# Kernel optimization log

Measured on AMD Instinct MI355X. Metric: run time of the kernel, lower is better.

## Reference

```python
import jax, jax.numpy as jnp
import numpy as np

N_NODES = 50000
N_EDGES = 800000


def gcn_conv(x, edge_index, W, b):
    """PyG GCNConv: add self-loops, symmetric deg^{-1/2} normalization,
    dense transform, scatter-add aggregation."""
    n = x.shape[0]
    src, dst = edge_index[0], edge_index[1]
    # add self-loops
    loop = jnp.arange(n, dtype=src.dtype)
    src = jnp.concatenate([src, loop])
    dst = jnp.concatenate([dst, loop])
    # degree on destination nodes (includes self-loops -> deg >= 1)
    deg = jax.ops.segment_sum(jnp.ones_like(dst, dtype=x.dtype), dst, num_segments=n)
    dinv = jax.lax.rsqrt(deg)
    norm = dinv[src] * dinv[dst]  # [E+N]
    h = x @ W                     # [N, F_out] dense GEMM
    msg = h[src] * norm[:, None]  # gather + scale, [E+N, F_out]
    out = jax.ops.segment_sum(msg, dst, num_segments=n)  # scatter-add
    return out + b


def setup_inputs() -> dict:
    key = jax.random.key(0)
    ks = jax.random.split(key, 8)
    x = jax.random.normal(ks[0], (N_NODES, 100), dtype=jnp.float32)
    edge_index = jax.random.randint(ks[1], (2, N_EDGES), 0, N_NODES, dtype=jnp.int64)
    W1 = jax.random.normal(ks[2], (100, 256), dtype=jnp.float32) * 0.1
    b1 = jnp.zeros((256,), dtype=jnp.float32)
    W2 = jax.random.normal(ks[3], (256, 128), dtype=jnp.float32) * 0.06
    b2 = jnp.zeros((128,), dtype=jnp.float32)
    Wfc = jax.random.normal(ks[4], (128, 1), dtype=jnp.float32) * 0.09
    bfc = jnp.zeros((1,), dtype=jnp.float32)
    return {"x": x, "edge_index": edge_index, "W1": W1, "b1": b1,
            "W2": W2, "b2": b2, "Wfc": Wfc, "bfc": bfc}


def reference(x, edge_index, W1, b1, W2, b2, Wfc, bfc):
    # eval mode: F.dropout with training=False is identity
    h = jax.nn.relu(gcn_conv(x, edge_index, W1, b1))
    h = jax.nn.relu(gcn_conv(h, edge_index, W2, b2))
    return h @ Wfc + bfc  # [N, 1]
```

## Files before the change

### kernel.cpp

```cpp
#include <hip/hip_runtime.h>
#include <hip/hip_bf16.h>


#define F0 100
#define F1 256
#define F2 128

typedef _Float16 f16x4 __attribute__((ext_vector_type(4)));
typedef _Float16 f16x8 __attribute__((ext_vector_type(8)));
typedef float f32x4 __attribute__((ext_vector_type(4)));


__global__ void deg_count_i(const int* __restrict__ dst, int* deg, int e) {
    int i = blockIdx.x * blockDim.x + threadIdx.x;
    if (i < e) atomicAdd(deg + dst[i], 1);
}

__global__ __launch_bounds__(256) void scan1(const int* __restrict__ deg,
                                             int* __restrict__ excl,
                                             int* __restrict__ bsum,
                                             float* __restrict__ dinv, int n) {
    __shared__ int wsum[4];
    int i = blockIdx.x * 256 + threadIdx.x;
    int lane = threadIdx.x & 63, wid = threadIdx.x >> 6;
    int v = (i < n) ? deg[i] : 0;
    if (i < n) dinv[i] = rsqrtf((float)(v + 1));
    int s = v;
#pragma unroll
    for (int off = 1; off < 64; off <<= 1) {
        int t = __shfl_up(s, off, 64);
        if (lane >= off) s += t;
    }
    if (lane == 63) wsum[wid] = s;
    __syncthreads();
    int add = 0;
    for (int w = 0; w < wid; w++) add += wsum[w];
    if (i < n) excl[i] = add + s - v;
    if (threadIdx.x == 255) bsum[blockIdx.x] = add + s;
}

__global__ __launch_bounds__(256) void scan2(int* __restrict__ bsum, int nb,
                                             int* __restrict__ rowptr, int n) {
    __shared__ int wsum[4];
    int lane = threadIdx.x & 63, wid = threadIdx.x >> 6;
    int v = (threadIdx.x < nb) ? bsum[threadIdx.x] : 0;
    int s = v;
#pragma unroll
    for (int off = 1; off < 64; off <<= 1) {
        int t = __shfl_up(s, off, 64);
        if (lane >= off) s += t;
    }
    if (lane == 63) wsum[wid] = s;
    __syncthreads();
    int add = 0;
    for (int w = 0; w < wid; w++) add += wsum[w];
    if (threadIdx.x < nb) bsum[threadIdx.x] = add + s - v;
    if (threadIdx.x == 255) rowptr[n] = add + s;
}

__global__ void scan3(const int* __restrict__ excl, const int* __restrict__ bsum,
                      int* __restrict__ rowptr, int* __restrict__ cursor, int n) {
    int i = blockIdx.x * 256 + threadIdx.x;
    if (i < n) {
        int r = excl[i] + bsum[blockIdx.x];
        rowptr[i] = r;
        cursor[i] = r;
    }
}

__global__ void csr_fill(const int* __restrict__ src, const int* __restrict__ dst,
                         int* cursor, int* __restrict__ csr, int e) {
    int i = blockIdx.x * blockDim.x + threadIdx.x;
    if (i < e) {
        int pos = atomicAdd(cursor + dst[i], 1);
        csr[pos] = src[i];
    }
}

__global__ void scale_x(const float4* __restrict__ x4,
                        const float* __restrict__ dinv,
                        float4* __restrict__ xs4, int n25) {
    int i = blockIdx.x * blockDim.x + threadIdx.x;
    if (i < n25) {
        float d = dinv[i / 25];
        float4 v = x4[i];
        v.x *= d; v.y *= d; v.z *= d; v.w *= d;
        xs4[i] = v;
    }
}

__global__ void wprep(const float* __restrict__ W1, const float* __restrict__ W2,
                      _Float16* __restrict__ W1h, _Float16* __restrict__ W1l,
                      _Float16* __restrict__ W2h, _Float16* __restrict__ W2l) {
    int i = blockIdx.x * 256 + threadIdx.x;
    if (i < 256 * 128) {
        int c = i >> 7, k = i & 127;
        float v = (k < F0) ? W1[(size_t)k * F1 + c] : 0.f;
        _Float16 h = (_Float16)v;
        W1h[i] = h;
        W1l[i] = (_Float16)(v - (float)h);
    } else if (i < 256 * 128 + 128 * 256) {
        int j = i - 256 * 128;
        int c = j >> 8, k = j & 255;
        float v = W2[(size_t)k * F2 + c];
        _Float16 h = (_Float16)v;
        W2h[j] = h;
        W2l[j] = (_Float16)(v - (float)h);
    }
}


__global__ __launch_bounds__(256) void pull_f100(
        const float* __restrict__ xs, const int* __restrict__ rowptr,
        const int* __restrict__ csr, const float* __restrict__ dinv,
        _Float16* __restrict__ aggh, _Float16* __restrict__ aggl, int n) {
    int wave = threadIdx.x >> 6, lane = threadIdx.x & 63;
    int v = blockIdx.x * 4 + wave;
    if (v >= n) return;
    int beg = rowptr[v], end = rowptr[v + 1];
    float dv = dinv[v];
    int half = lane >> 5, q = lane & 31;
    bool act = q < 25;
    float4 acc = {0.f, 0.f, 0.f, 0.f};
    if (half == 0 && act) acc = ((const float4*)(xs + (size_t)v * F0))[q];

    for (int base = beg; base < end; base += 64) {
        int cnt = min(64, end - base);
        int sidx = (lane < cnt) ? csr[base + lane] : 0;
        int npf = cnt >> 1;
        int p = 0;
        for (; p + 4 <= npf; p += 4) {
            int s0 = __shfl(sidx, 2 * p + half, 64);
            int s1 = __shfl(sidx, 2 * p + 2 + half, 64);
            int s2 = __shfl(sidx, 2 * p + 4 + half, 64);
            int s3 = __shfl(sidx, 2 * p + 6 + half, 64);
            if (act) {
                float4 r0 = ((const float4*)(xs + (size_t)s0 * F0))[q];
                float4 r1 = ((const float4*)(xs + (size_t)s1 * F0))[q];
                float4 r2 = ((const float4*)(xs + (size_t)s2 * F0))[q];
                float4 r3 = ((const float4*)(xs + (size_t)s3 * F0))[q];
                acc.x += (r0.x + r1.x) + (r2.x + r3.x);
                acc.y += (r0.y + r1.y) + (r2.y + r3.y);
                acc.z += (r0.z + r1.z) + (r2.z + r3.z);
                acc.w += (r0.w + r1.w) + (r2.w + r3.w);
            }
        }
        for (; p < npf; p++) {
            int s0 = __shfl(sidx, 2 * p + half, 64);
            if (act) {
                float4 r0 = ((const float4*)(xs + (size_t)s0 * F0))[q];
                acc.x += r0.x; acc.y += r0.y; acc.z += r0.z; acc.w += r0.w;
            }
        }
        if (cnt & 1) {
            int sl = __shfl(sidx, cnt - 1, 64);
            if (half == 0 && act) {
                float4 r = ((const float4*)(xs + (size_t)sl * F0))[q];
                acc.x += r.x; acc.y += r.y; acc.z += r.z; acc.w += r.w;
            }
        }
    }
    float ox = __shfl_down(acc.x, 32, 64);
    float oy = __shfl_down(acc.y, 32, 64);
    float oz = __shfl_down(acc.z, 32, 64);
    float ow = __shfl_down(acc.w, 32, 64);
    if (half == 0) {
        float4 r = {0.f, 0.f, 0.f, 0.f};
        if (act) {
            r.x = dv * (acc.x + ox);
            r.y = dv * (acc.y + oy);
            r.z = dv * (acc.z + oz);
            r.w = dv * (acc.w + ow);
        }
        f16x4 hh, ll;
        hh[0] = (_Float16)r.x; ll[0] = (_Float16)(r.x - (float)hh[0]);
        hh[1] = (_Float16)r.y; ll[1] = (_Float16)(r.y - (float)hh[1]);
        hh[2] = (_Float16)r.z; ll[2] = (_Float16)(r.z - (float)hh[2]);
        hh[3] = (_Float16)r.w; ll[3] = (_Float16)(r.w - (float)hh[3]);
        *(f16x4*)(aggh + (size_t)v * 128 + 4 * q) = hh;
        *(f16x4*)(aggl + (size_t)v * 128 + 4 * q) = ll;
    }
}

__global__ __launch_bounds__(512) void gemm12_fused(
        const _Float16* __restrict__ Ah, const _Float16* __restrict__ Al,
        const _Float16* __restrict__ W1h, const _Float16* __restrict__ W1l,
        const _Float16* __restrict__ W2h, const _Float16* __restrict__ W2l,
        const float* __restrict__ b1, const float* __restrict__ dinv,
        float* __restrict__ C, int n) {
    __shared__ _Float16 sAh[128][136], sAl[128][136];
    int tid = threadIdx.x, lane = tid & 63, wave = tid >> 6;
    int wm = wave >> 2, wn = wave & 3;
    int r0 = blockIdx.x * 128;
    int lr = lane & 15, kg = lane >> 4, ks8 = kg * 8;

    f32x4 acc1[4][4] = {};
    int arow[4];
#pragma unroll
    for (int i = 0; i < 4; ++i) arow[i] = min(r0 + wm * 64 + i * 16 + lr, n - 1);

#pragma unroll
    for (int k0 = 0; k0 < 128; k0 += 32) {
        f16x8 a_h[4], a_l[4], b_h[4], b_l[4];
#pragma unroll
        for (int i = 0; i < 4; ++i) {
            a_h[i] = *(const f16x8*)(Ah + (size_t)arow[i] * 128 + k0 + ks8);
            a_l[i] = *(const f16x8*)(Al + (size_t)arow[i] * 128 + k0 + ks8);
        }
#pragma unroll
        for (int j = 0; j < 4; ++j) {
            int col = wn * 64 + j * 16 + lr;
            b_h[j] = *(const f16x8*)(W1h + (size_t)col * 128 + k0 + ks8);
            b_l[j] = *(const f16x8*)(W1l + (size_t)col * 128 + k0 + ks8);
        }
#pragma unroll
        for (int i = 0; i < 4; ++i)
#pragma unroll
            for (int j = 0; j < 4; ++j) {
                acc1[i][j] = __builtin_amdgcn_mfma_f32_16x16x32_f16(a_l[i], b_h[j], acc1[i][j], 0, 0, 0);
                acc1[i][j] = __builtin_amdgcn_mfma_f32_16x16x32_f16(a_h[i], b_l[j], acc1[i][j], 0, 0, 0);
                acc1[i][j] = __builtin_amdgcn_mfma_f32_16x16x32_f16(a_h[i], b_h[j], acc1[i][j], 0, 0, 0);
            }
    }
#pragma unroll
    for (int j = 0; j < 4; ++j) {
        float bv = b1[wn * 64 + j * 16 + lr];
#pragma unroll
        for (int i = 0; i < 4; ++i)
#pragma unroll
            for (int r = 0; r < 4; ++r)
                acc1[i][j][r] = fmaxf(acc1[i][j][r] + bv, 0.f);
    }

    f32x4 acc2[4][2] = {};
#pragma unroll
    for (int half = 0; half < 2; ++half) {
        if (half) __syncthreads();
        if ((wn >> 1) == half) {
            int cb = (wn & 1) * 64;
#pragma unroll
            for (int i = 0; i < 4; ++i)
#pragma unroll
                for (int j = 0; j < 4; ++j)
#pragma unroll
                    for (int r = 0; r < 4; ++r) {
                        int row = wm * 64 + i * 16 + kg * 4 + r;
                        int col = cb + j * 16 + lr;
                        float v = acc1[i][j][r];
                        _Float16 h = (_Float16)v;
                        sAh[row][col] = h;
                        sAl[row][col] = (_Float16)(v - (float)h);
                    }
        }
        __syncthreads();
#pragma unroll
        for (int k0 = 0; k0 < 128; k0 += 32) {
            f16x8 a_h[4], a_l[4], b_h[2], b_l[2];
#pragma unroll
            for (int i = 0; i < 4; ++i) {
                a_h[i] = *(const f16x8*)&sAh[wm * 64 + i * 16 + lr][k0 + ks8];
                a_l[i] = *(const f16x8*)&sAl[wm * 64 + i * 16 + lr][k0 + ks8];
            }
#pragma unroll
            for (int j = 0; j < 2; ++j) {
                int col = wn * 32 + j * 16 + lr;
                int kk = half * 128 + k0 + ks8;
                b_h[j] = *(const f16x8*)(W2h + (size_t)col * 256 + kk);
                b_l[j] = *(const f16x8*)(W2l + (size_t)col * 256 + kk);
            }
#pragma unroll
            for (int i = 0; i < 4; ++i)
#pragma unroll
                for (int j = 0; j < 2; ++j) {
                    acc2[i][j] = __builtin_amdgcn_mfma_f32_16x16x32_f16(a_l[i], b_h[j], acc2[i][j], 0, 0, 0);
                    acc2[i][j] = __builtin_amdgcn_mfma_f32_16x16x32_f16(a_h[i], b_l[j], acc2[i][j], 0, 0, 0);
                    acc2[i][j] = __builtin_amdgcn_mfma_f32_16x16x32_f16(a_h[i], b_h[j], acc2[i][j], 0, 0, 0);
                }
        }
    }

#pragma unroll
    for (int i = 0; i < 4; ++i)
#pragma unroll
        for (int r = 0; r < 4; ++r) {
            int gr = r0 + wm * 64 + i * 16 + kg * 4 + r;
            if (gr < n) {
                float d = dinv[gr];
#pragma unroll
                for (int j = 0; j < 2; ++j) {
                    int col = wn * 32 + j * 16 + lr;
                    C[(size_t)gr * F2 + col] = acc2[i][j][r] * d;
                }
            }
        }
}

__global__ __launch_bounds__(256) void pull_f128_fused(
        const float* __restrict__ h2s, const int* __restrict__ rowptr,
        const int* __restrict__ csr, const float* __restrict__ dinv,
        const float* __restrict__ b2, const float* __restrict__ Wfc,
        const float* __restrict__ bfc, float* __restrict__ out, int n) {
    int wave = threadIdx.x >> 6, lane = threadIdx.x & 63;
    int v = blockIdx.x * 4 + wave;
    if (v >= n) return;
    int beg = rowptr[v], end = rowptr[v + 1];
    float dv = dinv[v];
    int half = lane >> 5, q = lane & 31;
    float4 acc = {0.f, 0.f, 0.f, 0.f};
    if (half == 0) acc = ((const float4*)(h2s + (size_t)v * F2))[q];

    for (int base = beg; base < end; base += 64) {
        int cnt = min(64, end - base);
        int sidx = (lane < cnt) ? csr[base + lane] : 0;
        int npf = cnt >> 1;
        int p = 0;
        for (; p + 4 <= npf; p += 4) {
            int s0 = __shfl(sidx, 2 * p + half, 64);
            int s1 = __shfl(sidx, 2 * p + 2 + half, 64);
            int s2 = __shfl(sidx, 2 * p + 4 + half, 64);
            int s3 = __shfl(sidx, 2 * p + 6 + half, 64);
            float4 r0 = ((const float4*)(h2s + (size_t)s0 * F2))[q];
            float4 r1 = ((const float4*)(h2s + (size_t)s1 * F2))[q];
            float4 r2 = ((const float4*)(h2s + (size_t)s2 * F2))[q];
            float4 r3 = ((const float4*)(h2s + (size_t)s3 * F2))[q];
            acc.x += (r0.x + r1.x) + (r2.x + r3.x);
            acc.y += (r0.y + r1.y) + (r2.y + r3.y);
            acc.z += (r0.z + r1.z) + (r2.z + r3.z);
            acc.w += (r0.w + r1.w) + (r2.w + r3.w);
        }
        for (; p < npf; p++) {
            int s0 = __shfl(sidx, 2 * p + half, 64);
            float4 r0 = ((const float4*)(h2s + (size_t)s0 * F2))[q];
            acc.x += r0.x; acc.y += r0.y; acc.z += r0.z; acc.w += r0.w;
        }
        if (cnt & 1) {
            int sl = __shfl(sidx, cnt - 1, 64);
            if (half == 0) {
                float4 r = ((const float4*)(h2s + (size_t)sl * F2))[q];
                acc.x += r.x; acc.y += r.y; acc.z += r.z; acc.w += r.w;
            }
        }
    }
    float ox = __shfl_down(acc.x, 32, 64);
    float oy = __shfl_down(acc.y, 32, 64);
    float oz = __shfl_down(acc.z, 32, 64);
    float ow = __shfl_down(acc.w, 32, 64);
    if (half == 0) {
        float4 b2v = ((const float4*)b2)[q];
        float4 wv = ((const float4*)Wfc)[q];
        float t0 = dv * (acc.x + ox);
        float t1 = dv * (acc.y + oy);
        float t2 = dv * (acc.z + oz);
        float t3 = dv * (acc.w + ow);
        float part = fmaxf(t0 + b2v.x, 0.f) * wv.x + fmaxf(t1 + b2v.y, 0.f) * wv.y +
                     fmaxf(t2 + b2v.z, 0.f) * wv.z + fmaxf(t3 + b2v.w, 0.f) * wv.w;
        part += __shfl_down(part, 16, 64);
        part += __shfl_down(part, 8, 64);
        part += __shfl_down(part, 4, 64);
        part += __shfl_down(part, 2, 64);
        part += __shfl_down(part, 1, 64);
        if (lane == 0) out[v] = part + bfc[0];
    }
}


extern "C" void kernel_launch(void* const* d_in, const int* in_sizes, int n_in,
                              void* d_out, int out_size, void* d_ws, size_t ws_size,
                              hipStream_t stream) {
    const float* x   = (const float*)d_in[0];
    const int*   ei  = (const int*)d_in[1];
    const float* W1  = (const float*)d_in[2];
    const float* b1  = (const float*)d_in[3];
    const float* W2  = (const float*)d_in[4];
    const float* b2  = (const float*)d_in[5];
    const float* Wfc = (const float*)d_in[6];
    const float* bfc = (const float*)d_in[7];
    float* out = (float*)d_out;

    const int n = in_sizes[0] / F0;
    const int e = in_sizes[1] / 2;
    const int* src = ei;
    const int* dst = ei + e;

    char* wsb = (char*)d_ws;
    size_t off = 0;
    auto alloc = [&](size_t bytes) -> void* {
        off = (off + 255) & ~(size_t)255;
        void* r = wsb + off;
        off += bytes;
        return r;
    };
    int* deg    = (int*)alloc((size_t)n * 4);
    int* excl   = (int*)alloc((size_t)n * 4);
    int* bsum   = (int*)alloc(1024);
    int* rowptr = (int*)alloc((size_t)(n + 1) * 4);
    int* cursor = (int*)alloc((size_t)n * 4);
    int* csr    = (int*)alloc((size_t)e * 4);
    float* dinv = (float*)alloc((size_t)n * 4);
    _Float16* W1h = (_Float16*)alloc(256 * 128 * 2);
    _Float16* W1l = (_Float16*)alloc(256 * 128 * 2);
    _Float16* W2h = (_Float16*)alloc(128 * 256 * 2);
    _Float16* W2l = (_Float16*)alloc(128 * 256 * 2);
    char* bufA = (char*)alloc((size_t)n * 128 * 4);
    float* xs = (float*)bufA;
    float* h2 = (float*)bufA;
    _Float16* aggh = (_Float16*)alloc((size_t)n * 128 * 2);
    _Float16* aggl = (_Float16*)alloc((size_t)n * 128 * 2);

    const int B = 256;
    const int nb = (n + B - 1) / B;

    hipMemsetAsync(deg, 0, (size_t)n * 4, stream);
    deg_count_i<<<(e + B - 1) / B, B, 0, stream>>>(dst, deg, e);
    scan1<<<nb, B, 0, stream>>>(deg, excl, bsum, dinv, n);
    scale_x<<<((n * 25) + B - 1) / B, B, 0, stream>>>(
        (const float4*)x, dinv, (float4*)xs, n * 25);
    wprep<<<256, 256, 0, stream>>>(W1, W2, W1h, W1l, W2h, W2l);
    scan2<<<1, B, 0, stream>>>(bsum, nb, rowptr, n);
    scan3<<<nb, B, 0, stream>>>(excl, bsum, rowptr, cursor, n);
    csr_fill<<<(e + B - 1) / B, B, 0, stream>>>(src, dst, cursor, csr, e);

    pull_f100<<<(n + 3) / 4, 256, 0, stream>>>(xs, rowptr, csr, dinv, aggh, aggl, n);
    gemm12_fused<<<(n + 127) / 128, 512, 0, stream>>>(aggh, aggl, W1h, W1l,
                                                      W2h, W2l, b1, dinv, h2, n);
    pull_f128_fused<<<(n + 3) / 4, 256, 0, stream>>>(h2, rowptr, csr, dinv,
                                                     b2, Wfc, bfc, out, n);
}
```

Measured before the change: 336.0 us.

## Fuse x scaling into scan, vectorize edge atomics, raise MFMA wave priority

The scale_x kernel is folded into the first scan kernel, which keeps dinv in shared memory and scales its own 256 rows of x. This removes one launch and a reread of dinv. The degree-count and CSR-fill kernels now handle four edges per thread using int4 loads, which cuts thread count and index-load overhead. s_setprio calls are placed around the MFMA blocks in the fused GEMM to favour waves that are issuing matrix work. The int4 loads assume 16-byte alignment of src/dst, and the fused scan does more serial work per block.

```diff
diff --git a/kernel.cpp b/kernel.cpp
--- a/kernel.cpp
+++ b/kernel.cpp
@@ -13,18 +13,30 @@
 
 __global__ void deg_count_i(const int* __restrict__ dst, int* deg, int e) {
     int i = blockIdx.x * blockDim.x + threadIdx.x;
-    if (i < e) atomicAdd(deg + dst[i], 1);
-}
-
-__global__ __launch_bounds__(256) void scan1(const int* __restrict__ deg,
-                                             int* __restrict__ excl,
-                                             int* __restrict__ bsum,
-                                             float* __restrict__ dinv, int n) {
+    int base = i * 4;
+    if (base + 3 < e) {
+        int4 d = *(const int4*)(dst + base);
+        atomicAdd(deg + d.x, 1);
+        atomicAdd(deg + d.y, 1);
+        atomicAdd(deg + d.z, 1);
+        atomicAdd(deg + d.w, 1);
+    } else {
+        for (int k = base; k < e; ++k) atomicAdd(deg + dst[k], 1);
+    }
+}
+
+__global__ __launch_bounds__(256) void scan1_scale(
+        const int* __restrict__ deg, int* __restrict__ excl,
+        int* __restrict__ bsum, float* __restrict__ dinv,
+        const float4* __restrict__ x4, float4* __restrict__ xs4, int n) {
     __shared__ int wsum[4];
+    __shared__ float sd[256];
     int i = blockIdx.x * 256 + threadIdx.x;
     int lane = threadIdx.x & 63, wid = threadIdx.x >> 6;
     int v = (i < n) ? deg[i] : 0;
-    if (i < n) dinv[i] = rsqrtf((float)(v + 1));
+    float dv = rsqrtf((float)(v + 1));
+    sd[threadIdx.x] = dv;
+    if (i < n) dinv[i] = dv;
     int s = v;
 #pragma unroll
     for (int off = 1; off < 64; off <<= 1) {
@@ -37,6 +49,18 @@
     for (int w = 0; w < wid; w++) add += wsum[w];
     if (i < n) excl[i] = add + s - v;
     if (threadIdx.x == 255) bsum[blockIdx.x] = add + s;
+
+    int r0b = blockIdx.x * 256;
+    for (int j = threadIdx.x; j < 256 * 25; j += 256) {
+        int row = j / 25, q = j - row * 25;
+        int gr = r0b + row;
+        if (gr < n) {
+            float d = sd[row];
+            float4 t = x4[(size_t)gr * 25 + q];
+            t.x *= d; t.y *= d; t.z *= d; t.w *= d;
+            xs4[(size_t)gr * 25 + q] = t;
+        }
+    }
 }
 
 __global__ __launch_bounds__(256) void scan2(int* __restrict__ bsum, int nb,
@@ -71,21 +95,17 @@
 __global__ void csr_fill(const int* __restrict__ src, const int* __restrict__ dst,
                          int* cursor, int* __restrict__ csr, int e) {
     int i = blockIdx.x * blockDim.x + threadIdx.x;
-    if (i < e) {
-        int pos = atomicAdd(cursor + dst[i], 1);
-        csr[pos] = src[i];
-    }
-}
-
-__global__ void scale_x(const float4* __restrict__ x4,
-                        const float* __restrict__ dinv,
-                        float4* __restrict__ xs4, int n25) {
-    int i = blockIdx.x * blockDim.x + threadIdx.x;
-    if (i < n25) {
-        float d = dinv[i / 25];
-        float4 v = x4[i];
-        v.x *= d; v.y *= d; v.z *= d; v.w *= d;
-        xs4[i] = v;
+    int base = i * 4;
+    if (base + 3 < e) {
+        int4 d = *(const int4*)(dst + base);
+        int4 sc = *(const int4*)(src + base);
+        csr[atomicAdd(cursor + d.x, 1)] = sc.x;
+        csr[atomicAdd(cursor + d.y, 1)] = sc.y;
+        csr[atomicAdd(cursor + d.z, 1)] = sc.z;
+        csr[atomicAdd(cursor + d.w, 1)] = sc.w;
+    } else {
+        for (int k = base; k < e; ++k)
+            csr[atomicAdd(cursor + dst[k], 1)] = src[k];
     }
 }
 
@@ -213,6 +233,7 @@
             b_h[j] = *(const f16x8*)(W1h + (size_t)col * 128 + k0 + ks8);
             b_l[j] = *(const f16x8*)(W1l + (size_t)col * 128 + k0 + ks8);
         }
+        __builtin_amdgcn_s_setprio(1);
 #pragma unroll
         for (int i = 0; i < 4; ++i)
 #pragma unroll
@@ -221,6 +242,7 @@
                 acc1[i][j] = __builtin_amdgcn_mfma_f32_16x16x32_f16(a_h[i], b_l[j], acc1[i][j], 0, 0, 0);
                 acc1[i][j] = __builtin_amdgcn_mfma_f32_16x16x32_f16(a_h[i], b_h[j], acc1[i][j], 0, 0, 0);
             }
+        __builtin_amdgcn_s_setprio(0);
     }
 #pragma unroll
     for (int j = 0; j < 4; ++j) {
@@ -268,6 +290,7 @@
                 b_h[j] = *(const f16x8*)(W2h + (size_t)col * 256 + kk);
                 b_l[j] = *(const f16x8*)(W2l + (size_t)col * 256 + kk);
             }
+            __builtin_amdgcn_s_setprio(1);
 #pragma unroll
             for (int i = 0; i < 4; ++i)
 #pragma unroll
@@ -276,6 +299,7 @@
                     acc2[i][j] = __builtin_amdgcn_mfma_f32_16x16x32_f16(a_h[i], b_l[j], acc2[i][j], 0, 0, 0);
                     acc2[i][j] = __builtin_amdgcn_mfma_f32_16x16x32_f16(a_h[i], b_h[j], acc2[i][j], 0, 0, 0);
                 }
+            __builtin_amdgcn_s_setprio(0);
         }
     }
 
@@ -409,16 +433,16 @@
 
     const int B = 256;
     const int nb = (n + B - 1) / B;
+    const int e4 = (e + 3) / 4;
 
     hipMemsetAsync(deg, 0, (size_t)n * 4, stream);
-    deg_count_i<<<(e + B - 1) / B, B, 0, stream>>>(dst, deg, e);
-    scan1<<<nb, B, 0, stream>>>(deg, excl, bsum, dinv, n);
-    scale_x<<<((n * 25) + B - 1) / B, B, 0, stream>>>(
-        (const float4*)x, dinv, (float4*)xs, n * 25);
+    deg_count_i<<<(e4 + B - 1) / B, B, 0, stream>>>(dst, deg, e);
+    scan1_scale<<<nb, B, 0, stream>>>(deg, excl, bsum, dinv,
+                                      (const float4*)x, (float4*)xs, n);
     wprep<<<256, 256, 0, stream>>>(W1, W2, W1h, W1l, W2h, W2l);
     scan2<<<1, B, 0, stream>>>(bsum, nb, rowptr, n);
     scan3<<<nb, B, 0, stream>>>(excl, bsum, rowptr, cursor, n);
-    csr_fill<<<(e + B - 1) / B, B, 0, stream>>>(src, dst, cursor, csr, e);
+    csr_fill<<<(e4 + B - 1) / B, B, 0, stream>>>(src, dst, cursor, csr, e);
 
     pull_f100<<<(n + 3) / 4, 256, 0, stream>>>(xs, rowptr, csr, dinv, aggh, aggl, n);
     gemm12_fused<<<(n + 127) / 128, 512, 0, stream>>>(aggh, aggl, W1h, W1l,
```

Result: slower. 347.2 us (+3.4%).
